# Kernel optimization log

Measured on AMD Instinct MI355X. Metric: run time of the kernel, lower is better.

The kernel has to match this reference:

```python
import jax, jax.numpy as jnp
import numpy as np

EPS = 1e-8  # torch CosineSimilarity default eps

def setup_inputs() -> dict:
    key = jax.random.key(0)
    kv, kt, k1, k2, k3, k4 = jax.random.split(key, 6)
    B, S = 16, 1024
    VD, TD, H = 1024, 768, 512
    visual_features = jax.random.normal(kv, (B, S, VD), dtype=jnp.float32)
    text_features = jax.random.normal(kt, (B, S, TD), dtype=jnp.float32)
    # nn.Linear params: weight [out, in], bias [out]
    Wv = jax.random.normal(k1, (H, VD), dtype=jnp.float32) * (1.0 / np.sqrt(VD))
    bv = jax.random.normal(k2, (H,), dtype=jnp.float32) * 0.01
    Wt = jax.random.normal(k3, (H, TD), dtype=jnp.float32) * (1.0 / np.sqrt(TD))
    bt = jax.random.normal(k4, (H,), dtype=jnp.float32) * 0.01
    return {"visual_features": visual_features, "text_features": text_features,
            "Wv": Wv, "bv": bv, "Wt": Wt, "bt": bt}

def reference(visual_features, text_features, Wv, bv, Wt, bt):
    # Linear projections
    v = jnp.einsum('bsd,hd->bsh', visual_features, Wv) + bv  # [B,S,H]
    t = jnp.einsum('bsd,hd->bsh', text_features, Wt) + bt    # [B,S,H]
    # Cosine similarity matrix via normalized batched GEMM
    # (algebraically equal to broadcasting CosineSimilarity over (B,S,S,H))
    dots = jnp.einsum('bih,bjh->bij', v, t)                   # [B,S,S]
    vn = jnp.linalg.norm(v, axis=-1)                          # [B,S]
    tn = jnp.linalg.norm(t, axis=-1)                          # [B,S]
    denom = jnp.maximum(vn[:, :, None] * tn[:, None, :], EPS)
    return dots / denom
```

## Files before the change

kernel.cpp:

```cpp
#include <hip/hip_runtime.h>
#include <hip/hip_bf16.h>

typedef __bf16 bf16x8 __attribute__((ext_vector_type(8)));
typedef __bf16 bf16x4 __attribute__((ext_vector_type(4)));
typedef float  f32x4  __attribute__((ext_vector_type(4)));

#define MFMA16(a, b, c) __builtin_amdgcn_mfma_f32_16x16x32_bf16((a), (b), (c), 0, 0, 0)

#define BATCH 16
#define SEQ   1024
#define VD    1024
#define TD    768
#define HDIM  512
#define MROWS (BATCH * SEQ)

typedef __attribute__((address_space(1))) const unsigned int gas_uint;
typedef __attribute__((address_space(3))) unsigned int las_uint;

__device__ __forceinline__ void async_copy16(const void* g, void* l) {
    __builtin_amdgcn_global_load_lds((gas_uint*)g, (las_uint*)l, 16, 0, 0);
}

__device__ __forceinline__ void stage_tile_bf16(const __bf16* __restrict__ src,
                                                size_t ld, int row0, int k0,
                                                __bf16* __restrict__ buf, int tid) {
#pragma unroll
    for (int i = 0; i < 4; ++i) {
        const int c = i * 256 + tid;
        const int r = c >> 3;
        const int g = (c & 7) ^ (r & 7);
        async_copy16(&src[(size_t)(row0 + r) * ld + k0 + g * 8],
                     &buf[(c & ~63) * 8]);
    }
}

__device__ __forceinline__ bf16x8 frag_read(const __bf16* __restrict__ buf,
                                            int r, int h, int fq) {
    return *reinterpret_cast<const bf16x8*>(&buf[(r * 8 + ((h * 4 + fq) ^ (r & 7))) * 8]);
}

#define NC_XV (BATCH * SEQ * VD / 4)
#define NC_XT (BATCH * SEQ * TD / 4)
#define NC_WV (HDIM * VD / 4)
#define NC_WT (HDIM * TD / 4)
#define NC_TOTAL (NC_XV + NC_XT + NC_WV + NC_WT)

__global__ __launch_bounds__(256) void conv_kernel(
    const float* __restrict__ Xv, const float* __restrict__ Xt,
    const float* __restrict__ Wv, const float* __restrict__ Wt,
    __bf16* __restrict__ Xvb, __bf16* __restrict__ Xtb,
    __bf16* __restrict__ Wvb, __bf16* __restrict__ Wtb) {
    int i = blockIdx.x * 256 + threadIdx.x;
    if (i >= NC_TOTAL) return;
    const float* src;
    __bf16* dst;
    if (i < NC_XV)                     { src = Xv; dst = Xvb; }
    else if ((i -= NC_XV) < NC_XT)     { src = Xt; dst = Xtb; }
    else if ((i -= NC_XT) < NC_WV)     { src = Wv; dst = Wvb; }
    else { i -= NC_WV;                   src = Wt; dst = Wtb; }
    const float4 x = reinterpret_cast<const float4*>(src)[i];
    bf16x4 p = {(__bf16)x.x, (__bf16)x.y, (__bf16)x.z, (__bf16)x.w};
    reinterpret_cast<bf16x4*>(dst)[i] = p;
}

__global__ __launch_bounds__(256) void proj_kernel(
    const __bf16* __restrict__ Xvb, const __bf16* __restrict__ Wvb, const float* __restrict__ bv_,
    const __bf16* __restrict__ Xtb, const __bf16* __restrict__ Wtb, const float* __restrict__ bt_,
    __bf16* __restrict__ vout, __bf16* __restrict__ tout,
    float* __restrict__ vn2, float* __restrict__ tn2)
{
    const int L     = blockIdx.x;
    const int mlow  = L & 7;
    const int n     = (L >> 3) & 3;
    const int mhigh = (L >> 5) & 15;
    const int z     = L >> 9;
    const int m0    = (mhigh * 8 + mlow) * 128;
    const int n0    = n * 128;

    const __bf16* X; const __bf16* Wb; const float* bias; __bf16* out; float* n2; int K;
    if (z == 0) { X = Xvb; Wb = Wvb; bias = bv_; out = vout; n2 = vn2; K = VD; }
    else        { X = Xtb; Wb = Wtb; bias = bt_; out = tout; n2 = tn2; K = TD; }

    __shared__ __bf16 As[2][128 * 64];
    __shared__ __bf16 Bs[2][128 * 64];

    const int tid  = threadIdx.x;
    const int lane = tid & 63;
    const int wave = tid >> 6;
    const int wr   = wave >> 1;
    const int wc   = wave & 1;
    const int fr   = lane & 15;
    const int fq   = lane >> 4;

    f32x4 acc[4][4] = {};
    const int nk = K >> 6;

    stage_tile_bf16(X,  K, m0, 0, As[0], tid);
    stage_tile_bf16(Wb, K, n0, 0, Bs[0], tid);
    __syncthreads();

    for (int ki = 0; ki < nk; ++ki) {
        if (ki + 1 < nk) {
            const int kk = (ki + 1) << 6;
            stage_tile_bf16(X,  K, m0, kk, As[(ki + 1) & 1], tid);
            stage_tile_bf16(Wb, K, n0, kk, Bs[(ki + 1) & 1], tid);
        }
        const __bf16* Ab = As[ki & 1];
        const __bf16* Bb = Bs[ki & 1];
#pragma unroll
        for (int h = 0; h < 2; ++h) {
            bf16x8 a[4], b[4];
#pragma unroll
            for (int tm = 0; tm < 4; ++tm)
                a[tm] = frag_read(Ab, wr * 64 + tm * 16 + fr, h, fq);
#pragma unroll
            for (int tn = 0; tn < 4; ++tn)
                b[tn] = frag_read(Bb, wc * 64 + tn * 16 + fr, h, fq);
#pragma unroll
            for (int tm = 0; tm < 4; ++tm)
#pragma unroll
                for (int tn = 0; tn < 4; ++tn)
                    acc[tm][tn] = MFMA16(a[tm], b[tn], acc[tm][tn]);
        }
        __syncthreads();
    }

    float bc[4];
#pragma unroll
    for (int tn = 0; tn < 4; ++tn)
        bc[tn] = bias[n0 + wc * 64 + tn * 16 + fr];

#pragma unroll
    for (int tm = 0; tm < 4; ++tm) {
        const int rowb = m0 + wr * 64 + tm * 16 + fq * 4;
#pragma unroll
        for (int r = 0; r < 4; ++r) {
            float s = 0.f;
#pragma unroll
            for (int tn = 0; tn < 4; ++tn) {
                const float e = acc[tm][tn][r] + bc[tn];
                out[(size_t)(rowb + r) * HDIM + n0 + wc * 64 + tn * 16 + fr] = (__bf16)e;
                s = fmaf(e, e, s);
            }
            s += __shfl_xor(s, 1);
            s += __shfl_xor(s, 2);
            s += __shfl_xor(s, 4);
            s += __shfl_xor(s, 8);
            if (fr == 0) atomicAdd(&n2[rowb + r], s);
        }
    }
}

__global__ __launch_bounds__(256) void dots_kernel(const __bf16* __restrict__ v,
                                                   const __bf16* __restrict__ t,
                                                   const float* __restrict__ vn2,
                                                   const float* __restrict__ tn2,
                                                   float* __restrict__ out) {
    __shared__ __bf16 As[2][128 * 64];
    __shared__ __bf16 Bs[2][128 * 64];

    const int L  = blockIdx.x;
    const int b  = (L & 7) + ((L >> 9) << 3);
    const int j0 = ((L >> 3) & 7) * 128;
    const int i0 = ((L >> 6) & 7) * 128;

    const __bf16* vb = v + (size_t)b * SEQ * HDIM;
    const __bf16* tb = t + (size_t)b * SEQ * HDIM;

    const int tid  = threadIdx.x;
    const int lane = tid & 63;
    const int wave = tid >> 6;
    const int wr   = wave >> 1;
    const int wc   = wave & 1;
    const int fr   = lane & 15;
    const int fq   = lane >> 4;

    f32x4 acc[4][4] = {};
    const int nk = HDIM >> 6;

    stage_tile_bf16(vb, HDIM, i0, 0, As[0], tid);
    stage_tile_bf16(tb, HDIM, j0, 0, Bs[0], tid);
    __syncthreads();

    for (int ki = 0; ki < nk; ++ki) {
        if (ki + 1 < nk) {
            const int kk = (ki + 1) << 6;
            stage_tile_bf16(vb, HDIM, i0, kk, As[(ki + 1) & 1], tid);
            stage_tile_bf16(tb, HDIM, j0, kk, Bs[(ki + 1) & 1], tid);
        }
        const __bf16* Ab = As[ki & 1];
        const __bf16* Bb = Bs[ki & 1];
#pragma unroll
        for (int h = 0; h < 2; ++h) {
            bf16x8 a[4], bfr[4];
#pragma unroll
            for (int tm = 0; tm < 4; ++tm)
                a[tm] = frag_read(Ab, wr * 64 + tm * 16 + fr, h, fq);
#pragma unroll
            for (int tn = 0; tn < 4; ++tn)
                bfr[tn] = frag_read(Bb, wc * 64 + tn * 16 + fr, h, fq);
#pragma unroll
            for (int tm = 0; tm < 4; ++tm)
#pragma unroll
                for (int tn = 0; tn < 4; ++tn)
                    acc[tm][tn] = MFMA16(a[tm], bfr[tn], acc[tm][tn]);
        }
        __syncthreads();
    }

    float vr2[16];
#pragma unroll
    for (int tm = 0; tm < 4; ++tm)
#pragma unroll
        for (int r = 0; r < 4; ++r)
            vr2[tm * 4 + r] = vn2[b * SEQ + i0 + wr * 64 + tm * 16 + fq * 4 + r];

    float* outb = out + ((size_t)b << 20);
#pragma unroll
    for (int tn = 0; tn < 4; ++tn) {
        const int j     = j0 + wc * 64 + tn * 16 + fr;
        const float tj2 = tn2[b * SEQ + j];
#pragma unroll
        for (int tm = 0; tm < 4; ++tm) {
            const int ib = i0 + wr * 64 + tm * 16 + fq * 4;
#pragma unroll
            for (int r = 0; r < 4; ++r) {
                const float denom = fmaxf(sqrtf(vr2[tm * 4 + r] * tj2), 1e-8f);
                outb[(size_t)(ib + r) * SEQ + j] = acc[tm][tn][r] * __builtin_amdgcn_rcpf(denom);
            }
        }
    }
}

extern "C" void kernel_launch(void* const* d_in, const int* in_sizes, int n_in,
                              void* d_out, int out_size, void* d_ws, size_t ws_size,
                              hipStream_t stream) {
    const float* Xv = (const float*)d_in[0];
    const float* Xt = (const float*)d_in[1];
    const float* Wv = (const float*)d_in[2];
    const float* bv = (const float*)d_in[3];
    const float* Wt = (const float*)d_in[4];
    const float* bt = (const float*)d_in[5];
    float* out = (float*)d_out;

    char* ws = (char*)d_ws;
    size_t off = 0;
    __bf16* v   = (__bf16*)(ws + off); off += (size_t)MROWS * HDIM * 2;
    __bf16* t   = (__bf16*)(ws + off); off += (size_t)MROWS * HDIM * 2;
    __bf16* Xvb = (__bf16*)(ws + off); off += (size_t)MROWS * VD * 2;
    __bf16* Xtb = (__bf16*)(ws + off); off += (size_t)MROWS * TD * 2;
    __bf16* Wvb = (__bf16*)(ws + off); off += (size_t)HDIM * VD * 2;
    __bf16* Wtb = (__bf16*)(ws + off); off += (size_t)HDIM * TD * 2;
    float*  vn2 = (float*)(ws + off);  off += (size_t)MROWS * 4;
    float*  tn2 = (float*)(ws + off);  off += (size_t)MROWS * 4;

    hipMemsetAsync(vn2, 0, (size_t)2 * MROWS * 4, stream);

    conv_kernel<<<(NC_TOTAL + 255) / 256, 256, 0, stream>>>(Xv, Xt, Wv, Wt, Xvb, Xtb, Wvb, Wtb);

    proj_kernel<<<1024, 256, 0, stream>>>(Xvb, Wvb, bv, Xtb, Wtb, bt, v, t, vn2, tn2);

    dots_kernel<<<1024, 256, 0, stream>>>(v, t, vn2, tn2, out);
}
```

Baseline: 248.3 us.

## Warp-specialize GEMM kernels with producer loader waves and LDS flag sync

Both GEMM kernels now run 6 waves per block. Two producer waves issue async global-to-LDS copies and four consumer waves run the MFMA loop. The producers and consumers coordinate through shared-memory ready/done counters with spin-waits in place of block-wide barriers. The aim is to overlap tile loading with compute and remove the __syncthreads stalls. In exchange, each block has more threads and pays spin/sleep polling overhead. The waitcnt immediate and the cross-wave LDS visibility of async copies under workgroup-scope atomics could also raise correctness or ordering risks.

```diff
diff --git a/kernel.cpp b/kernel.cpp
--- a/kernel.cpp
+++ b/kernel.cpp
@@ -14,6 +14,8 @@
 #define HDIM  512
 #define MROWS (BATCH * SEQ)
 
+#define WAIT_VM0 0x0F70
+
 typedef __attribute__((address_space(1))) const unsigned int gas_uint;
 typedef __attribute__((address_space(3))) unsigned int las_uint;
 
@@ -21,22 +23,30 @@
     __builtin_amdgcn_global_load_lds((gas_uint*)g, (las_uint*)l, 16, 0, 0);
 }
 
-__device__ __forceinline__ void stage_tile_bf16(const __bf16* __restrict__ src,
+__device__ __forceinline__ void stage_tile_wave(const __bf16* __restrict__ src,
                                                 size_t ld, int row0, int k0,
-                                                __bf16* __restrict__ buf, int tid) {
-#pragma unroll
-    for (int i = 0; i < 4; ++i) {
-        const int c = i * 256 + tid;
+                                                __bf16* __restrict__ buf, int lane) {
+#pragma unroll
+    for (int i = 0; i < 16; ++i) {
+        const int c = i * 64 + lane;
         const int r = c >> 3;
         const int g = (c & 7) ^ (r & 7);
-        async_copy16(&src[(size_t)(row0 + r) * ld + k0 + g * 8],
-                     &buf[(c & ~63) * 8]);
+        async_copy16(&src[(size_t)(row0 + r) * ld + k0 + g * 8], &buf[i * 512]);
     }
 }
 
 __device__ __forceinline__ bf16x8 frag_read(const __bf16* __restrict__ buf,
                                             int r, int h, int fq) {
     return *reinterpret_cast<const bf16x8*>(&buf[(r * 8 + ((h * 4 + fq) ^ (r & 7))) * 8]);
+}
+
+__device__ __forceinline__ void spin_until(int* p, int target) {
+    while (__hip_atomic_load(p, __ATOMIC_ACQUIRE, __HIP_MEMORY_SCOPE_WORKGROUP) < target)
+        __builtin_amdgcn_s_sleep(1);
+}
+__device__ __forceinline__ void signal(int* p, int lane) {
+    if (lane == 0)
+        __hip_atomic_fetch_add(p, 1, __ATOMIC_RELEASE, __HIP_MEMORY_SCOPE_WORKGROUP);
 }
 
 #define NC_XV (BATCH * SEQ * VD / 4)
@@ -54,16 +64,16 @@
     if (i >= NC_TOTAL) return;
     const float* src;
     __bf16* dst;
-    if (i < NC_XV)                     { src = Xv; dst = Xvb; }
-    else if ((i -= NC_XV) < NC_XT)     { src = Xt; dst = Xtb; }
-    else if ((i -= NC_XT) < NC_WV)     { src = Wv; dst = Wvb; }
-    else { i -= NC_WV;                   src = Wt; dst = Wtb; }
+    if (i < NC_XV)                 { src = Xv; dst = Xvb; }
+    else if ((i -= NC_XV) < NC_XT) { src = Xt; dst = Xtb; }
+    else if ((i -= NC_XT) < NC_WV) { src = Wv; dst = Wvb; }
+    else { i -= NC_WV;               src = Wt; dst = Wtb; }
     const float4 x = reinterpret_cast<const float4*>(src)[i];
     bf16x4 p = {(__bf16)x.x, (__bf16)x.y, (__bf16)x.z, (__bf16)x.w};
     reinterpret_cast<bf16x4*>(dst)[i] = p;
 }
 
-__global__ __launch_bounds__(256) void proj_kernel(
+__global__ __launch_bounds__(384) void proj_kernel(
     const __bf16* __restrict__ Xvb, const __bf16* __restrict__ Wvb, const float* __restrict__ bv_,
     const __bf16* __restrict__ Xtb, const __bf16* __restrict__ Wtb, const float* __restrict__ bt_,
     __bf16* __restrict__ vout, __bf16* __restrict__ tout,
@@ -83,81 +93,90 @@
 
     __shared__ __bf16 As[2][128 * 64];
     __shared__ __bf16 Bs[2][128 * 64];
+    __shared__ int ready[16];
+    __shared__ int done[16];
 
     const int tid  = threadIdx.x;
     const int lane = tid & 63;
     const int wave = tid >> 6;
-    const int wr   = wave >> 1;
-    const int wc   = wave & 1;
-    const int fr   = lane & 15;
-    const int fq   = lane >> 4;
-
-    f32x4 acc[4][4] = {};
+    if (tid < 16) { ready[tid] = 0; done[tid] = 0; }
+    __syncthreads();
+
     const int nk = K >> 6;
 
-    stage_tile_bf16(X,  K, m0, 0, As[0], tid);
-    stage_tile_bf16(Wb, K, n0, 0, Bs[0], tid);
-    __syncthreads();
-
-    for (int ki = 0; ki < nk; ++ki) {
-        if (ki + 1 < nk) {
-            const int kk = (ki + 1) << 6;
-            stage_tile_bf16(X,  K, m0, kk, As[(ki + 1) & 1], tid);
-            stage_tile_bf16(Wb, K, n0, kk, Bs[(ki + 1) & 1], tid);
-        }
-        const __bf16* Ab = As[ki & 1];
-        const __bf16* Bb = Bs[ki & 1];
-#pragma unroll
-        for (int h = 0; h < 2; ++h) {
-            bf16x8 a[4], b[4];
-#pragma unroll
-            for (int tm = 0; tm < 4; ++tm)
-                a[tm] = frag_read(Ab, wr * 64 + tm * 16 + fr, h, fq);
-#pragma unroll
-            for (int tn = 0; tn < 4; ++tn)
-                b[tn] = frag_read(Bb, wc * 64 + tn * 16 + fr, h, fq);
-#pragma unroll
-            for (int tm = 0; tm < 4; ++tm)
+    if (wave < 2) {
+        const __bf16* src = (wave == 0) ? X : Wb;
+        const int row0    = (wave == 0) ? m0 : n0;
+        for (int s = 0; s < nk; ++s) {
+            if (s >= 2) spin_until(&done[s - 2], 4);
+            stage_tile_wave(src, K, row0, s << 6, (wave == 0) ? As[s & 1] : Bs[s & 1], lane);
+            __builtin_amdgcn_s_waitcnt(WAIT_VM0);
+            signal(&ready[s], lane);
+        }
+    } else {
+        const int cw = wave - 2;
+        const int wr = cw >> 1, wc = cw & 1;
+        const int fr = lane & 15, fq = lane >> 4;
+        f32x4 acc[4][4] = {};
+
+        for (int s = 0; s < nk; ++s) {
+            spin_until(&ready[s], 2);
+            const __bf16* Ab = As[s & 1];
+            const __bf16* Bb = Bs[s & 1];
+#pragma unroll
+            for (int h = 0; h < 2; ++h) {
+                bf16x8 a[4], b[4];
+#pragma unroll
+                for (int tm = 0; tm < 4; ++tm)
+                    a[tm] = frag_read(Ab, wr * 64 + tm * 16 + fr, h, fq);
 #pragma unroll
                 for (int tn = 0; tn < 4; ++tn)
-                    acc[tm][tn] = MFMA16(a[tm], b[tn], acc[tm][tn]);
-        }
-        __syncthreads();
+                    b[tn] = frag_read(Bb, wc * 64 + tn * 16 + fr, h, fq);
+#pragma unroll
+                for (int tm = 0; tm < 4; ++tm)
+#pragma unroll
+                    for (int tn = 0; tn < 4; ++tn)
+                        acc[tm][tn] = MFMA16(a[tm], b[tn], acc[tm][tn]);
+            }
+            signal(&done[s], lane);
+        }
+
+        float bc[4];
+#pragma unroll
+        for (int tn = 0; tn < 4; ++tn)
+            bc[tn] = bias[n0 + wc * 64 + tn * 16 + fr];
+
+#pragma unroll
+        for (int tm = 0; tm < 4; ++tm) {
+            const int rowb = m0 + wr * 64 + tm * 16 + fq * 4;
+#pragma unroll
+            for (int r = 0; r < 4; ++r) {
+                float s = 0.f;
+#pragma unroll
+                for (int tn = 0; tn < 4; ++tn) {
+                    const float e = acc[tm][tn][r] + bc[tn];
+                    out[(size_t)(rowb + r) * HDIM + n0 + wc * 64 + tn * 16 + fr] = (__bf16)e;
+                    s = fmaf(e, e, s);
+                }
+                s += __shfl_xor(s, 1);
+                s += __shfl_xor(s, 2);
+                s += __shfl_xor(s, 4);
+                s += __shfl_xor(s, 8);
+                if (fr == 0) atomicAdd(&n2[rowb + r], s);
+            }
+        }
     }
-
-    float bc[4];
-#pragma unroll
-    for (int tn = 0; tn < 4; ++tn)
-        bc[tn] = bias[n0 + wc * 64 + tn * 16 + fr];
-
-#pragma unroll
-    for (int tm = 0; tm < 4; ++tm) {
-        const int rowb = m0 + wr * 64 + tm * 16 + fq * 4;
-#pragma unroll
-        for (int r = 0; r < 4; ++r) {
-            float s = 0.f;
-#pragma unroll
-            for (int tn = 0; tn < 4; ++tn) {
-                const float e = acc[tm][tn][r] + bc[tn];
-                out[(size_t)(rowb + r) * HDIM + n0 + wc * 64 + tn * 16 + fr] = (__bf16)e;
-                s = fmaf(e, e, s);
-            }
-            s += __shfl_xor(s, 1);
-            s += __shfl_xor(s, 2);
-            s += __shfl_xor(s, 4);
-            s += __shfl_xor(s, 8);
-            if (fr == 0) atomicAdd(&n2[rowb + r], s);
-        }
-    }
-}
-
-__global__ __launch_bounds__(256) void dots_kernel(const __bf16* __restrict__ v,
+}
+
+__global__ __launch_bounds__(384) void dots_kernel(const __bf16* __restrict__ v,
                                                    const __bf16* __restrict__ t,
                                                    const float* __restrict__ vn2,
                                                    const float* __restrict__ tn2,
                                                    float* __restrict__ out) {
     __shared__ __bf16 As[2][128 * 64];
     __shared__ __bf16 Bs[2][128 * 64];
+    __shared__ int ready[16];
+    __shared__ int done[16];
 
     const int L  = blockIdx.x;
     const int b  = (L & 7) + ((L >> 9) << 3);
@@ -170,63 +189,68 @@
     const int tid  = threadIdx.x;
     const int lane = tid & 63;
     const int wave = tid >> 6;
-    const int wr   = wave >> 1;
-    const int wc   = wave & 1;
-    const int fr   = lane & 15;
-    const int fq   = lane >> 4;
-
-    f32x4 acc[4][4] = {};
+    if (tid < 16) { ready[tid] = 0; done[tid] = 0; }
+    __syncthreads();
+
     const int nk = HDIM >> 6;
 
-    stage_tile_bf16(vb, HDIM, i0, 0, As[0], tid);
-    stage_tile_bf16(tb, HDIM, j0, 0, Bs[0], tid);
-    __syncthreads();
-
-    for (int ki = 0; ki < nk; ++ki) {
-        if (ki + 1 < nk) {
-            const int kk = (ki + 1) << 6;
-            stage_tile_bf16(vb, HDIM, i0, kk, As[(ki + 1) & 1], tid);
-            stage_tile_bf16(tb, HDIM, j0, kk, Bs[(ki + 1) & 1], tid);
-        }
-        const __bf16* Ab = As[ki & 1];
-        const __bf16* Bb = Bs[ki & 1];
-#pragma unroll
-        for (int h = 0; h < 2; ++h) {
-            bf16x8 a[4], bfr[4];
-#pragma unroll
-            for (int tm = 0; tm < 4; ++tm)
-                a[tm] = frag_read(Ab, wr * 64 + tm * 16 + fr, h, fq);
-#pragma unroll
-            for (int tn = 0; tn < 4; ++tn)
-                bfr[tn] = frag_read(Bb, wc * 64 + tn * 16 + fr, h, fq);
-#pragma unroll
-            for (int tm = 0; tm < 4; ++tm)
+    if (wave < 2) {
+        const __bf16* src = (wave == 0) ? vb : tb;
+        const int row0    = (wave == 0) ? i0 : j0;
+        for (int s = 0; s < nk; ++s) {
+            if (s >= 2) spin_until(&done[s - 2], 4);
+            stage_tile_wave(src, HDIM, row0, s << 6, (wave == 0) ? As[s & 1] : Bs[s & 1], lane);
+            __builtin_amdgcn_s_waitcnt(WAIT_VM0);
+            signal(&ready[s], lane);
+        }
+    } else {
+        const int cw = wave - 2;
+        const int wr = cw >> 1, wc = cw & 1;
+        const int fr = lane & 15, fq = lane >> 4;
+        f32x4 acc[4][4] = {};
+
+        for (int s = 0; s < nk; ++s) {
+            spin_until(&ready[s], 2);
+            const __bf16* Ab = As[s & 1];
+            const __bf16* Bb = Bs[s & 1];
+#pragma unroll
+            for (int h = 0; h < 2; ++h) {
+                bf16x8 a[4], bfr[4];
+#pragma unroll
+                for (int tm = 0; tm < 4; ++tm)
+                    a[tm] = frag_read(Ab, wr * 64 + tm * 16 + fr, h, fq);
 #pragma unroll
                 for (int tn = 0; tn < 4; ++tn)
-                    acc[tm][tn] = MFMA16(a[tm], bfr[tn], acc[tm][tn]);
-        }
-        __syncthreads();
-    }
-
-    float vr2[16];
-#pragma unroll
-    for (int tm = 0; tm < 4; ++tm)
-#pragma unroll
-        for (int r = 0; r < 4; ++r)
-            vr2[tm * 4 + r] = vn2[b * SEQ + i0 + wr * 64 + tm * 16 + fq * 4 + r];
-
-    float* outb = out + ((size_t)b << 20);
-#pragma unroll
-    for (int tn = 0; tn < 4; ++tn) {
-        const int j     = j0 + wc * 64 + tn * 16 + fr;
-        const float tj2 = tn2[b * SEQ + j];
-#pragma unroll
-        for (int tm = 0; tm < 4; ++tm) {
-            const int ib = i0 + wr * 64 + tm * 16 + fq * 4;
-#pragma unroll
-            for (int r = 0; r < 4; ++r) {
-                const float denom = fmaxf(sqrtf(vr2[tm * 4 + r] * tj2), 1e-8f);
-                outb[(size_t)(ib + r) * SEQ + j] = acc[tm][tn][r] * __builtin_amdgcn_rcpf(denom);
+                    bfr[tn] = frag_read(Bb, wc * 64 + tn * 16 + fr, h, fq);
+#pragma unroll
+                for (int tm = 0; tm < 4; ++tm)
+#pragma unroll
+                    for (int tn = 0; tn < 4; ++tn)
+                        acc[tm][tn] = MFMA16(a[tm], bfr[tn], acc[tm][tn]);
+            }
+            signal(&done[s], lane);
+        }
+
+        float vr2[16];
+#pragma unroll
+        for (int tm = 0; tm < 4; ++tm)
+#pragma unroll
+            for (int r = 0; r < 4; ++r)
+                vr2[tm * 4 + r] = vn2[b * SEQ + i0 + wr * 64 + tm * 16 + fq * 4 + r];
+
+        float* outb = out + ((size_t)b << 20);
+#pragma unroll
+        for (int tn = 0; tn < 4; ++tn) {
+            const int j     = j0 + wc * 64 + tn * 16 + fr;
+            const float tj2 = tn2[b * SEQ + j];
+#pragma unroll
+            for (int tm = 0; tm < 4; ++tm) {
+                const int ib = i0 + wr * 64 + tm * 16 + fq * 4;
+#pragma unroll
+                for (int r = 0; r < 4; ++r) {
+                    const float denom = fmaxf(sqrtf(vr2[tm * 4 + r] * tj2), 1e-8f);
+                    outb[(size_t)(ib + r) * SEQ + j] = acc[tm][tn][r] * __builtin_amdgcn_rcpf(denom);
+                }
             }
         }
     }
@@ -258,7 +282,7 @@
 
     conv_kernel<<<(NC_TOTAL + 255) / 256, 256, 0, stream>>>(Xv, Xt, Wv, Wt, Xvb, Xtb, Wvb, Wtb);
 
-    proj_kernel<<<1024, 256, 0, stream>>>(Xvb, Wvb, bv, Xtb, Wtb, bt, v, t, vn2, tn2);
-
-    dots_kernel<<<1024, 256, 0, stream>>>(v, t, vn2, tn2, out);
-}
+    proj_kernel<<<1024, 384, 0, stream>>>(Xvb, Wvb, bv, Xtb, Wtb, bt, v, t, vn2, tn2);
+
+    dots_kernel<<<1024, 384, 0, stream>>>(v, t, vn2, tn2, out);
+}
```

Measured after the change: 252.0 us. About the same (+1.5%).
